# Optimization experiments

Hardware: AMD Instinct MI355X
Metric: run time of the kernel (lower is better)

Reference implementation:

```python
import jax, jax.numpy as jnp
import numpy as np
import math

SR = 16000
FFT = 1024
WIN = 640
HOP = 320
NMEL = 40
NCEP = 13
B = 1024
NS = 16000
F_MIN = 0.0
F_MAX = 8000.0
LIFT_L = 22.0
DELTA_N = 2


def _linear_to_mel_weight_matrix(num_mel, num_spec_bins, sr, fmin, fmax):
    # Exact replica of tf.signal.linear_to_mel_weight_matrix (HTK mel scale).
    def hz_to_mel(f):
        return 1127.0 * np.log1p(np.asarray(f, np.float64) / 700.0)
    nyquist = sr / 2.0
    lin_freqs = np.linspace(0.0, nyquist, num_spec_bins)
    spec_mel = hz_to_mel(lin_freqs[1:])[:, None]          # drop DC bin
    edges = np.linspace(hz_to_mel(fmin), hz_to_mel(fmax), num_mel + 2)
    lower, center, upper = edges[:-2], edges[1:-1], edges[2:]
    lower_slope = (spec_mel - lower) / (center - lower)
    upper_slope = (upper - spec_mel) / (upper - center)
    w = np.maximum(0.0, np.minimum(lower_slope, upper_slope))
    w = np.pad(w, ((1, 0), (0, 0)))                       # re-add zero DC row
    return w.astype(np.float32)


def setup_inputs() -> dict:
    key = jax.random.key(0)
    waveforms = jax.random.normal(key, (B, NS), dtype=jnp.float32)
    mel_fb = jnp.asarray(_linear_to_mel_weight_matrix(NMEL, FFT // 2 + 1, SR, F_MIN, F_MAX))
    return {"waveforms": waveforms, "mel_fb": mel_fb}


def _delta(feat, N):
    # feat: (B, T, C). Replicate-pad N frames at both ends, then weighted
    # sliding-window sum with weights k in [-N..N] (vectorized, no map_fn).
    T = feat.shape[1]
    denom = 2.0 * sum(float(k * k) for k in range(1, N + 1))
    padded = jnp.concatenate(
        [jnp.repeat(feat[:, :1, :], N, axis=1), feat,
         jnp.repeat(feat[:, -1:, :], N, axis=1)], axis=1)
    acc = jnp.zeros_like(feat)
    for k in range(-N, N + 1):
        if k != 0:
            acc = acc + float(k) * padded[:, N + k:N + k + T, :]
    return acc / denom


def reference(waveforms, mel_fb):
    # --- STFT (tf.signal.stft: periodic Hann, no pad_end, zero-pad to FFT) ---
    n = jnp.arange(WIN, dtype=jnp.float32)
    window = 0.5 - 0.5 * jnp.cos(2.0 * math.pi * n / WIN)
    num_frames = 1 + (NS - WIN) // HOP                    # 49
    idx = jnp.arange(num_frames)[:, None] * HOP + jnp.arange(WIN)[None, :]
    frames = waveforms[:, idx] * window
    frames = jnp.pad(frames, ((0, 0), (0, 0), (0, FFT - WIN)))
    spec = jnp.abs(jnp.fft.rfft(frames, n=FFT, axis=-1))  # (B, T, 513)

    # --- mel + log ---
    log_mel = jnp.log(spec @ mel_fb + 1e-6)               # (B, T, NMEL)

    # --- MFCC: DCT-II scaled by rsqrt(2*NMEL), keep first NCEP coeffs ---
    m = jnp.arange(NMEL, dtype=jnp.float32)[:, None]
    k = jnp.arange(NCEP, dtype=jnp.float32)[None, :]
    dct_mat = 2.0 * jnp.cos(math.pi * (2.0 * m + 1.0) * k / (2.0 * NMEL))
    mfccs = (log_mel @ dct_mat) * (1.0 / math.sqrt(2.0 * NMEL))

    # --- liftering ---
    c = jnp.arange(NCEP, dtype=jnp.float32)
    lift = 1.0 + (LIFT_L / 2.0) * jnp.sin(math.pi * c / LIFT_L)
    mfccs = mfccs * lift

    # --- deltas and delta-deltas ---
    d1 = _delta(mfccs, DELTA_N)
    d2 = _delta(d1, DELTA_N)
    out = jnp.concatenate([mfccs, d1, d2], axis=2)        # (B, T, 3*NCEP)
    return out[..., None]                                 # (B, T, 39, 1)
```

## Files before the change

### kernel.cpp

```cpp
#include <hip/hip_runtime.h>
#include <math.h>

#define NMEL   40
#define NCEP   13
#define BATCH  1024
#define NSAMP  16000
#define NFRAME 49
#define PI_F   3.14159265358979323846f

#define WS_WIN  0
#define WS_R    640
#define WS_DT   1664
#define WS_BT   2184
#define WS_TOT  15240

typedef _Float16 half8 __attribute__((ext_vector_type(8)));
typedef __fp16   fp16x2 __attribute__((ext_vector_type(2)));
typedef float f32x4 __attribute__((ext_vector_type(4)));

#define FFT_SB() __builtin_amdgcn_sched_barrier(0x77)

#define BFLY(i0, i1, wr, wi) {                        \
    float tr = zr[i0] - zr[i1], ti = zi[i0] - zi[i1]; \
    zr[i0] += zr[i1]; zi[i0] += zi[i1];               \
    zr[i1] = tr*(wr) - ti*(wi);                       \
    zi[i1] = tr*(wi) + ti*(wr); }

__device__ __forceinline__ unsigned pk_f16(float a, float b) {
    fp16x2 h = __builtin_amdgcn_cvt_pkrtz(a, b);
    union { fp16x2 h; unsigned u; } cvt; cvt.h = h;
    return cvt.u;
}

__global__ __launch_bounds__(256) void mfcc_prep(
    const float* __restrict__ mel_fb, float* __restrict__ ws)
{
    const int idx = blockIdx.x * 256 + threadIdx.x;

    _Float16* bt = (_Float16*)(ws + WS_BT);
    for (int i = idx; i < 48 * 544; i += 64 * 256) {
        int n = i / 544, k = i - n * 544;
        float v = (n < NMEL && k < 513) ? mel_fb[k * NMEL + n] : 0.0f;
        bt[i] = (_Float16)v;
    }

    if (idx < 640 + 512 + 520) {
        int i = idx;
        if (i < 640) {
            ws[WS_WIN + i] = 0.5f - 0.5f * cosf(2.0f * PI_F * (float)i / 640.0f);
        } else if (i < 1152) {
            int k = i - 640;
            float s, c;
            sincosf(-2.0f * PI_F * (float)k / 1024.0f, &s, &c);
            ((float2*)(ws + WS_R))[k] = make_float2(c, s);
        } else {
            int j = i - 1152;
            int m = j / 13, c0 = j - m * 13;
            float d    = 2.0f * cosf(PI_F * (2.0f * m + 1.0f) * (float)c0 / 80.0f);
            float lift = 1.0f + 11.0f * sinf(PI_F * (float)c0 / 22.0f);
            ws[WS_DT + j] = d * 0.11180339887498949f * lift;
        }
    }
}

__device__ __forceinline__ void ldFrame(float2 (&x)[5], const float* __restrict__ wave,
                                        int frame, int L)
{
    const int b = frame / NFRAME;
    const int f = frame - b * NFRAME;
    const float2* xp = (const float2*)(wave + (size_t)b * NSAMP + (size_t)f * 320);
    #pragma unroll
    for (int j = 0; j < 5; ++j) x[j] = xp[L + 64 * j];
}

__device__ __forceinline__ void phaseI(float (&zr)[8], float (&zi)[8],
    const float2 (&xv)[5], const float2 (&winv)[5],
    const float2 (&twA)[4], const float2 (&twB)[2], const float2 twC)
{
    #pragma unroll
    for (int j = 0; j < 8; ++j) { zr[j] = 0.0f; zi[j] = 0.0f; }
    #pragma unroll
    for (int j = 0; j < 5; ++j) { zr[j] = xv[j].x * winv[j].x; zi[j] = xv[j].y * winv[j].y; }
    #pragma unroll
    for (int j = 0; j < 4; ++j) BFLY(j, j + 4, twA[j].x, twA[j].y);
    #pragma unroll
    for (int g = 0; g < 8; g += 4) {
        #pragma unroll
        for (int j = 0; j < 2; ++j) BFLY(g + j, g + j + 2, twB[j].x, twB[j].y);
    }
    #pragma unroll
    for (int i0 = 0; i0 < 8; i0 += 2) BFLY(i0, i0 + 1, twC.x, twC.y);
}

__device__ __forceinline__ void phaseII(float (&zr)[8], float (&zi)[8],
    const float4 (&q)[4],
    const float2 (&twD)[4], const float2 (&twE)[2], const float2 twF)
{
    zr[0] = q[0].x; zi[0] = q[0].y; zr[1] = q[0].z; zi[1] = q[0].w;
    zr[2] = q[1].x; zi[2] = q[1].y; zr[3] = q[1].z; zi[3] = q[1].w;
    zr[4] = q[2].x; zi[4] = q[2].y; zr[5] = q[2].z; zi[5] = q[2].w;
    zr[6] = q[3].x; zi[6] = q[3].y; zr[7] = q[3].z; zi[7] = q[3].w;
    #pragma unroll
    for (int j = 0; j < 4; ++j) BFLY(j, j + 4, twD[j].x, twD[j].y);
    #pragma unroll
    for (int g = 0; g < 8; g += 4) {
        #pragma unroll
        for (int j = 0; j < 2; ++j) BFLY(g + j, g + j + 2, twE[j].x, twE[j].y);
    }
    #pragma unroll
    for (int i0 = 0; i0 < 8; i0 += 2) BFLY(i0, i0 + 1, twF.x, twF.y);
}

__device__ __forceinline__ void phaseIII(float (&zr)[8], float (&zi)[8],
    const float4 (&q)[4])
{
    zr[0] = q[0].x; zi[0] = q[0].y; zr[1] = q[0].z; zi[1] = q[0].w;
    zr[2] = q[1].x; zi[2] = q[1].y; zr[3] = q[1].z; zi[3] = q[1].w;
    zr[4] = q[2].x; zi[4] = q[2].y; zr[5] = q[2].z; zi[5] = q[2].w;
    zr[6] = q[3].x; zi[6] = q[3].y; zr[7] = q[3].z; zi[7] = q[3].w;
    const float C = 0.70710678118654752f;
    const float w8r[4] = { 1.0f,  C, 0.0f, -C };
    const float w8i[4] = { 0.0f, -C, -1.0f, -C };
    #pragma unroll
    for (int j = 0; j < 4; ++j) BFLY(j, j + 4, w8r[j], w8i[j]);
    #pragma unroll
    for (int g = 0; g < 8; g += 4) {
        BFLY(g + 0, g + 2, 1.0f, 0.0f);
        BFLY(g + 1, g + 3, 0.0f, -1.0f);
    }
    #pragma unroll
    for (int i0 = 0; i0 < 8; i0 += 2) BFLY(i0, i0 + 1, 1.0f, 0.0f);
}

__device__ __forceinline__ void wrEx1(float2* Z, const float (&zr)[8], const float (&zi)[8],
                                      int s, int a)
{
    #pragma unroll
    for (int j = 0; j < 8; ++j) Z[80 * j + 10 * s + a] = make_float2(zr[j], zi[j]);
}

__device__ __forceinline__ void wrEx2(float2* Z, const float (&zr)[8], const float (&zi)[8],
                                      int s, int a)
{
    #pragma unroll
    for (int j = 0; j < 8; ++j) Z[80 * a + 10 * j + s] = make_float2(zr[j], zi[j]);
}

__device__ __forceinline__ void wrEx3(float2* Z, const float (&zr)[8], const float (&zi)[8],
                                      int u)
{
    const int rev3t[8] = { 0, 4, 2, 6, 1, 5, 3, 7 };
    #pragma unroll
    for (int j = 0; j < 8; ++j) Z[80 * rev3t[j] + u] = make_float2(zr[j], zi[j]);
}

__device__ __forceinline__ void rdEx(const float2* Z, int L, float4 (&q)[4])
{
    q[0] = *(const float4*)&Z[10 * L + 0];
    q[1] = *(const float4*)&Z[10 * L + 2];
    q[2] = *(const float4*)&Z[10 * L + 4];
    q[3] = *(const float4*)&Z[10 * L + 6];
}

__device__ __forceinline__ void rdMag(const float2* Z, int L,
    float4 (&aq)[4], float4 (&tq)[4], float2& b0)
{
    aq[0] = *(const float4*)&Z[10 * L + 0];
    aq[1] = *(const float4*)&Z[10 * L + 2];
    aq[2] = *(const float4*)&Z[10 * L + 4];
    aq[3] = *(const float4*)&Z[10 * L + 6];
    tq[0] = *(const float4*)&Z[630 - 10 * L + 0];
    tq[1] = *(const float4*)&Z[630 - 10 * L + 2];
    tq[2] = *(const float4*)&Z[630 - 10 * L + 4];
    tq[3] = *(const float4*)&Z[630 - 10 * L + 6];
    b0    = Z[640 - 10 * L];
}

__device__ __forceinline__ void magPhase(const float4 (&aq)[4], const float4 (&tq)[4],
    const float2 b0, const float2 (&twS)[8], const int L, uint4& mgpo, float& m512o)
{
    float Ax[8], Ay[8], Bx[8], By[8];
    Ax[0] = aq[0].x; Ay[0] = aq[0].y; Ax[1] = aq[0].z; Ay[1] = aq[0].w;
    Ax[2] = aq[1].x; Ay[2] = aq[1].y; Ax[3] = aq[1].z; Ay[3] = aq[1].w;
    Ax[4] = aq[2].x; Ay[4] = aq[2].y; Ax[5] = aq[2].z; Ay[5] = aq[2].w;
    Ax[6] = aq[3].x; Ay[6] = aq[3].y; Ax[7] = aq[3].z; Ay[7] = aq[3].w;
    Bx[0] = b0.x;    By[0] = b0.y;
    Bx[7] = tq[0].z; By[7] = tq[0].w;
    Bx[6] = tq[1].x; By[6] = tq[1].y;
    Bx[5] = tq[1].z; By[5] = tq[1].w;
    Bx[4] = tq[2].x; By[4] = tq[2].y;
    Bx[3] = tq[2].z; By[3] = tq[2].w;
    Bx[2] = tq[3].x; By[2] = tq[3].y;
    Bx[1] = tq[3].z; By[1] = tq[3].w;
    float mg[8];
    #pragma unroll
    for (int j = 0; j < 8; ++j) {
        float xer = 0.5f * (Ax[j] + Bx[j]), xei = 0.5f * (Ay[j] - By[j]);
        float xo  = 0.5f * (Ay[j] + By[j]), xoi = -0.5f * (Ax[j] - Bx[j]);
        float xr = xer + twS[j].x * xo - twS[j].y * xoi;
        float xi = xei + twS[j].x * xoi + twS[j].y * xo;
        mg[j] = __builtin_amdgcn_sqrtf(xr * xr + xi * xi);
    }
    if (L == 0) {
        mg[0]  = fabsf(Ax[0] + Ay[0]);
        m512o  = fabsf(Ax[0] - Ay[0]);
    }
    mgpo.x = pk_f16(mg[0], mg[1]);
    mgpo.y = pk_f16(mg[2], mg[3]);
    mgpo.z = pk_f16(mg[4], mg[5]);
    mgpo.w = pk_f16(mg[6], mg[7]);
}

__global__ __launch_bounds__(256) void mfcc_stage1(
    const float* __restrict__ wave, const float* __restrict__ ws,
    float* __restrict__ out)
{
    __shared__ __align__(16) char smem[4 * 640 * 8 + 16];
    char* smemc = smem;
    _Float16* lm = (_Float16*)(smem + 16 * 1104);

    const int tid = threadIdx.x;
    const int wv  = tid >> 6;
    const int L   = tid & 63;
    const int s   = L & 7;
    const int a   = L >> 3;

    float2* Z = (float2*)smem + wv * 640;
    const float2* R   = (const float2*)(ws + WS_R);
    const float2* win = (const float2*)(ws + WS_WIN);

    float2 twA[4], twB[2], twC, twD[4], twE[2], twF, twS[8], winv[5];
    #pragma unroll
    for (int j = 0; j < 4; ++j) twA[j] = R[2 * (L + 64 * j)];
    #pragma unroll
    for (int j = 0; j < 2; ++j) twB[j] = R[4 * (L + 64 * j)];
    twC = R[8 * L];
    #pragma unroll
    for (int j = 0; j < 4; ++j) twD[j] = R[128 * j + 16 * s];
    #pragma unroll
    for (int j = 0; j < 2; ++j) twE[j] = R[256 * j + 32 * s];
    twF = R[64 * s];
    #pragma unroll
    for (int j = 0; j < 8; ++j) twS[j] = R[8 * L + j];
    #pragma unroll
    for (int j = 0; j < 5; ++j) winv[j] = win[L + 64 * j];

    const int r6 = (int)(__brev((unsigned)L) >> 26);
    const int u  = r6 + 2 * (r6 >> 3);

    uint4 mgp0, mgp1, mgp2, mgp3;
    float m5120 = 0.0f, m5121 = 0.0f, m5122 = 0.0f, m5123 = 0.0f;

    const int fbase = blockIdx.x * 16 + wv * 4;

    float2 xA[5], xB[5];
    ldFrame(xA, wave, fbase + 0, L);
    ldFrame(xB, wave, fbase + 1, L);

    #pragma unroll 1
    for (int p = 0; p < 2; ++p) {
        float2 xA2[5], xB2[5];
        if (p == 0) {
            ldFrame(xA2, wave, fbase + 2, L);
            ldFrame(xB2, wave, fbase + 3, L);
        }

        float zrA[8], ziA[8], zrB[8], ziB[8];
        float4 qA[4], qB[4];

        phaseI(zrA, ziA, xA, winv, twA, twB, twC);
        FFT_SB();
        wrEx1(Z, zrA, ziA, s, a);
        FFT_SB();
        rdEx(Z, L, qA);
        FFT_SB();
        phaseI(zrB, ziB, xB, winv, twA, twB, twC);
        wrEx1(Z, zrB, ziB, s, a);
        FFT_SB();
        rdEx(Z, L, qB);
        FFT_SB();

        phaseII(zrA, ziA, qA, twD, twE, twF);
        wrEx2(Z, zrA, ziA, s, a);
        FFT_SB();
        rdEx(Z, L, qA);
        FFT_SB();
        phaseII(zrB, ziB, qB, twD, twE, twF);
        wrEx2(Z, zrB, ziB, s, a);
        FFT_SB();
        rdEx(Z, L, qB);
        FFT_SB();

        phaseIII(zrA, ziA, qA);
        wrEx3(Z, zrA, ziA, u);
        FFT_SB();
        float4 aqA[4], tqA[4]; float2 b0A;
        rdMag(Z, L, aqA, tqA, b0A);
        FFT_SB();
        phaseIII(zrB, ziB, qB);
        wrEx3(Z, zrB, ziB, u);
        FFT_SB();
        float4 aqB[4], tqB[4]; float2 b0B;
        rdMag(Z, L, aqB, tqB, b0B);
        FFT_SB();

        uint4 mgA, mgB;
        float mA = 0.0f, mB = 0.0f;
        magPhase(aqA, tqA, b0A, twS, L, mgA, mA);
        magPhase(aqB, tqB, b0B, twS, L, mgB, mB);
        FFT_SB();

        mgp0 = mgp2;  mgp1 = mgp3;  mgp2 = mgA;  mgp3 = mgB;
        m5120 = m5122; m5121 = m5123; m5122 = mA; m5123 = mB;

        if (p == 0) {
            #pragma unroll
            for (int j = 0; j < 5; ++j) { xA[j] = xA2[j]; xB[j] = xB2[j]; }
        }
    }

    __syncthreads();
    {
        const int row = wv * 4;
        *(uint4*)(smemc + (row + 0) * 1104 + 16 * L) = mgp0;
        *(uint4*)(smemc + (row + 1) * 1104 + 16 * L) = mgp1;
        *(uint4*)(smemc + (row + 2) * 1104 + 16 * L) = mgp2;
        *(uint4*)(smemc + (row + 3) * 1104 + 16 * L) = mgp3;
        if (L < 20) {
            unsigned v0 = (L == 0) ? pk_f16(m5120, 0.0f) : 0u;
            unsigned v1 = (L == 0) ? pk_f16(m5121, 0.0f) : 0u;
            unsigned v2 = (L == 0) ? pk_f16(m5122, 0.0f) : 0u;
            unsigned v3 = (L == 0) ? pk_f16(m5123, 0.0f) : 0u;
            *(unsigned*)(smemc + (row + 0) * 1104 + 1024 + 4 * L) = v0;
            *(unsigned*)(smemc + (row + 1) * 1104 + 1024 + 4 * L) = v1;
            *(unsigned*)(smemc + (row + 2) * 1104 + 1024 + 4 * L) = v2;
            *(unsigned*)(smemc + (row + 3) * 1104 + 1024 + 4 * L) = v3;
        }
    }
    __syncthreads();

    if (wv < 3) {
        const int nl = L & 15, q = L >> 4;
        const char* ap = smemc + nl * 1104 + q * 16;
        const _Float16* btp = (const _Float16*)(ws + WS_BT)
                              + (size_t)(wv * 16 + nl) * 544 + q * 8;
        f32x4 acc = {0.0f, 0.0f, 0.0f, 0.0f};
        #pragma unroll
        for (int kk = 0; kk < 17; ++kk) {
            half8 av = *(const half8*)(ap + kk * 64);
            half8 bv = *(const half8*)(btp + kk * 32);
            acc = __builtin_amdgcn_mfma_f32_16x16x32_f16(av, bv, acc, 0, 0, 0);
        }
        const int mel = wv * 16 + nl;
        if (mel < NMEL) {
            #pragma unroll
            for (int r = 0; r < 4; ++r) {
                int fl = q * 4 + r;
                lm[fl * NMEL + mel] = (_Float16)__logf(acc[r] + 1e-6f);
            }
        }
    }
    __syncthreads();

    if (tid < 16 * NCEP) {
        const int fl = tid / NCEP, c = tid - fl * NCEP;
        float acc = 0.0f;
        #pragma unroll
        for (int m = 0; m < NMEL; ++m)
            acc += (float)lm[fl * NMEL + m] * ws[WS_DT + m * 13 + c];
        out[(size_t)(blockIdx.x * 16 + fl) * (3 * NCEP) + c] = acc;
    }
}

__global__ __launch_bounds__(128) void mfcc_stage2(float* __restrict__ out)
{
    __shared__ float x [NFRAME * NCEP];
    __shared__ float d1[NFRAME * NCEP];

    const int b = blockIdx.x;
    const int tid = threadIdx.x;
    const int TC = NFRAME * NCEP;

    for (int i = tid; i < TC; i += 128) {
        const int t = i / NCEP, c = i - t * NCEP;
        x[i] = out[((size_t)b * NFRAME + t) * (3 * NCEP) + c];
    }
    __syncthreads();

    for (int i = tid; i < TC; i += 128) {
        const int t = i / NCEP, c = i - t * NCEP;
        float acc = 0.0f;
        #pragma unroll
        for (int k = -2; k <= 2; ++k) {
            if (k == 0) continue;
            int tt = t + k;
            tt = tt < 0 ? 0 : (tt > NFRAME - 1 ? NFRAME - 1 : tt);
            acc += (float)k * x[tt * NCEP + c];
        }
        d1[i] = acc * 0.1f;
    }
    __syncthreads();

    for (int i = tid; i < TC; i += 128) {
        const int t = i / NCEP, c = i - t * NCEP;
        float acc = 0.0f;
        #pragma unroll
        for (int k = -2; k <= 2; ++k) {
            if (k == 0) continue;
            int tt = t + k;
            tt = tt < 0 ? 0 : (tt > NFRAME - 1 ? NFRAME - 1 : tt);
            acc += (float)k * d1[tt * NCEP + c];
        }
        const size_t base = ((size_t)b * NFRAME + t) * (3 * NCEP);
        out[base +     NCEP + c] = d1[i];
        out[base + 2 * NCEP + c] = acc * 0.1f;
    }
}

extern "C" void kernel_launch(void* const* d_in, const int* in_sizes, int n_in,
                              void* d_out, int out_size, void* d_ws, size_t ws_size,
                              hipStream_t stream)
{
    const float* wave   = (const float*)d_in[0];
    const float* mel_fb = (const float*)d_in[1];
    float* out = (float*)d_out;
    float* ws  = (float*)d_ws;

    mfcc_prep<<<64, 256, 0, stream>>>(mel_fb, ws);
    mfcc_stage1<<<(BATCH * NFRAME) / 16, 256, 0, stream>>>(wave, ws, out);
    mfcc_stage2<<<BATCH, 128, 0, stream>>>(out);
}
```

Measured before the change: 152.3 us.

## Compute FFT twiddles on the fly and move next-frame prefetch later

Stops preloading the stage B/C/D/E/F and split twiddles from the workspace table into registers. They are now recomputed inside each phase with the hardware sin/cos instructions on revolution arguments. The prefetch of the next two frames now loads straight into the current frame registers once phase I of frame B is done, so the extra xA2/xB2 buffers and their copy go away. Together these cut live VGPRs and global twiddle loads, at the cost of many extra transcendental instructions per FFT and lower twiddle accuracy from the approximate hardware sin/cos.

```diff
diff --git a/kernel.cpp b/kernel.cpp
--- a/kernel.cpp
+++ b/kernel.cpp
@@ -14,6 +14,13 @@
 #define WS_BT   2184
 #define WS_TOT  15240
 
+#define INV16    0.0625f
+#define INV32    0.03125f
+#define INV64    0.015625f
+#define INV128   0.0078125f
+#define INV256   0.00390625f
+#define INV1024  0.0009765625f
+
 typedef _Float16 half8 __attribute__((ext_vector_type(8)));
 typedef __fp16   fp16x2 __attribute__((ext_vector_type(2)));
 typedef float f32x4 __attribute__((ext_vector_type(4)));
@@ -30,6 +37,10 @@
     fp16x2 h = __builtin_amdgcn_cvt_pkrtz(a, b);
     union { fp16x2 h; unsigned u; } cvt; cvt.h = h;
     return cvt.u;
+}
+
+__device__ __forceinline__ float2 twid(float rev) {
+    return make_float2(__builtin_amdgcn_cosf(rev), __builtin_amdgcn_sinf(rev));
 }
 
 __global__ __launch_bounds__(256) void mfcc_prep(
@@ -75,8 +86,12 @@
 
 __device__ __forceinline__ void phaseI(float (&zr)[8], float (&zi)[8],
     const float2 (&xv)[5], const float2 (&winv)[5],
-    const float2 (&twA)[4], const float2 (&twB)[2], const float2 twC)
-{
+    const float2 (&twA)[4], const int L)
+{
+    const float bb = -(float)L * INV256;
+    float2 twB[2] = { twid(bb), twid(bb - 0.25f) };
+    float2 twC    = twid(-(float)L * INV128);
+
     #pragma unroll
     for (int j = 0; j < 8; ++j) { zr[j] = 0.0f; zi[j] = 0.0f; }
     #pragma unroll
@@ -93,9 +108,14 @@
 }
 
 __device__ __forceinline__ void phaseII(float (&zr)[8], float (&zi)[8],
-    const float4 (&q)[4],
-    const float2 (&twD)[4], const float2 (&twE)[2], const float2 twF)
-{
+    const float4 (&q)[4], const int s)
+{
+    const float d0 = -(float)s * INV64;
+    float2 twD[4] = { twid(d0), twid(d0 - 0.125f), twid(d0 - 0.25f), twid(d0 - 0.375f) };
+    const float e0 = -(float)s * INV32;
+    float2 twE[2] = { twid(e0), twid(e0 - 0.25f) };
+    float2 twF    = twid(-(float)s * INV16);
+
     zr[0] = q[0].x; zi[0] = q[0].y; zr[1] = q[0].z; zi[1] = q[0].w;
     zr[2] = q[1].x; zi[2] = q[1].y; zr[3] = q[1].z; zi[3] = q[1].w;
     zr[4] = q[2].x; zi[4] = q[2].y; zr[5] = q[2].z; zi[5] = q[2].w;
@@ -177,7 +197,7 @@
 }
 
 __device__ __forceinline__ void magPhase(const float4 (&aq)[4], const float4 (&tq)[4],
-    const float2 b0, const float2 (&twS)[8], const int L, uint4& mgpo, float& m512o)
+    const float2 b0, const int L, uint4& mgpo, float& m512o)
 {
     float Ax[8], Ay[8], Bx[8], By[8];
     Ax[0] = aq[0].x; Ay[0] = aq[0].y; Ax[1] = aq[0].z; Ay[1] = aq[0].w;
@@ -192,13 +212,15 @@
     Bx[3] = tq[2].z; By[3] = tq[2].w;
     Bx[2] = tq[3].x; By[2] = tq[3].y;
     Bx[1] = tq[3].z; By[1] = tq[3].w;
+    const float s0 = -(float)L * INV128;
     float mg[8];
     #pragma unroll
     for (int j = 0; j < 8; ++j) {
+        float2 tws = twid(s0 - (float)j * INV1024);
         float xer = 0.5f * (Ax[j] + Bx[j]), xei = 0.5f * (Ay[j] - By[j]);
         float xo  = 0.5f * (Ay[j] + By[j]), xoi = -0.5f * (Ax[j] - Bx[j]);
-        float xr = xer + twS[j].x * xo - twS[j].y * xoi;
-        float xi = xei + twS[j].x * xoi + twS[j].y * xo;
+        float xr = xer + tws.x * xo - tws.y * xoi;
+        float xi = xei + tws.x * xoi + tws.y * xo;
         mg[j] = __builtin_amdgcn_sqrtf(xr * xr + xi * xi);
     }
     if (L == 0) {
@@ -229,19 +251,9 @@
     const float2* R   = (const float2*)(ws + WS_R);
     const float2* win = (const float2*)(ws + WS_WIN);
 
-    float2 twA[4], twB[2], twC, twD[4], twE[2], twF, twS[8], winv[5];
+    float2 twA[4], winv[5];
     #pragma unroll
     for (int j = 0; j < 4; ++j) twA[j] = R[2 * (L + 64 * j)];
-    #pragma unroll
-    for (int j = 0; j < 2; ++j) twB[j] = R[4 * (L + 64 * j)];
-    twC = R[8 * L];
-    #pragma unroll
-    for (int j = 0; j < 4; ++j) twD[j] = R[128 * j + 16 * s];
-    #pragma unroll
-    for (int j = 0; j < 2; ++j) twE[j] = R[256 * j + 32 * s];
-    twF = R[64 * s];
-    #pragma unroll
-    for (int j = 0; j < 8; ++j) twS[j] = R[8 * L + j];
     #pragma unroll
     for (int j = 0; j < 5; ++j) winv[j] = win[L + 64 * j];
 
@@ -259,33 +271,31 @@
 
     #pragma unroll 1
     for (int p = 0; p < 2; ++p) {
-        float2 xA2[5], xB2[5];
-        if (p == 0) {
-            ldFrame(xA2, wave, fbase + 2, L);
-            ldFrame(xB2, wave, fbase + 3, L);
-        }
-
         float zrA[8], ziA[8], zrB[8], ziB[8];
         float4 qA[4], qB[4];
 
-        phaseI(zrA, ziA, xA, winv, twA, twB, twC);
+        phaseI(zrA, ziA, xA, winv, twA, L);
         FFT_SB();
         wrEx1(Z, zrA, ziA, s, a);
         FFT_SB();
         rdEx(Z, L, qA);
         FFT_SB();
-        phaseI(zrB, ziB, xB, winv, twA, twB, twC);
+        phaseI(zrB, ziB, xB, winv, twA, L);
         wrEx1(Z, zrB, ziB, s, a);
         FFT_SB();
+        if (p == 0) {
+            ldFrame(xA, wave, fbase + 2, L);
+            ldFrame(xB, wave, fbase + 3, L);
+        }
         rdEx(Z, L, qB);
         FFT_SB();
 
-        phaseII(zrA, ziA, qA, twD, twE, twF);
+        phaseII(zrA, ziA, qA, s);
         wrEx2(Z, zrA, ziA, s, a);
         FFT_SB();
         rdEx(Z, L, qA);
         FFT_SB();
-        phaseII(zrB, ziB, qB, twD, twE, twF);
+        phaseII(zrB, ziB, qB, s);
         wrEx2(Z, zrB, ziB, s, a);
         FFT_SB();
         rdEx(Z, L, qB);
@@ -306,17 +316,12 @@
 
         uint4 mgA, mgB;
         float mA = 0.0f, mB = 0.0f;
-        magPhase(aqA, tqA, b0A, twS, L, mgA, mA);
-        magPhase(aqB, tqB, b0B, twS, L, mgB, mB);
+        magPhase(aqA, tqA, b0A, L, mgA, mA);
+        magPhase(aqB, tqB, b0B, L, mgB, mB);
         FFT_SB();
 
         mgp0 = mgp2;  mgp1 = mgp3;  mgp2 = mgA;  mgp3 = mgB;
         m5120 = m5122; m5121 = m5123; m5122 = mA; m5123 = mB;
-
-        if (p == 0) {
-            #pragma unroll
-            for (int j = 0; j < 5; ++j) { xA[j] = xA2[j]; xB[j] = xB2[j]; }
-        }
     }
 
     __syncthreads();
```

Result: no change. 149.7 us (-1.7%).
